# Optimization experiments

Measured on AMD Instinct MI355X. Metric: run time of the kernel, lower is better.

The kernel has to match this reference:

```python
import jax, jax.numpy as jnp
import numpy as np

N = 50000
E = 800000
IN_F, HID, OUT_F = 512, 256, 64
KEEP = 0.5  # Dropout(0.5)


def setup_inputs() -> dict:
    key = jax.random.key(0)
    ks = jax.random.split(key, 7)
    X = jax.random.normal(ks[0], (N, IN_F), dtype=jnp.float32)
    # Xavier-uniform-style init for the two layer weights
    lim1 = float(np.sqrt(6.0 / (IN_F + HID)))
    lim2 = float(np.sqrt(6.0 / (HID + OUT_F)))
    W1 = jax.random.uniform(ks[1], (IN_F, HID), jnp.float32, -lim1, lim1)
    W2 = jax.random.uniform(ks[2], (HID, OUT_F), jnp.float32, -lim2, lim2)
    a_row = jnp.sort(jax.random.randint(ks[3], (E,), 0, N)).astype(jnp.int64)
    a_col = jax.random.randint(ks[4], (E,), 0, N).astype(jnp.int64)
    a_val = jax.random.uniform(ks[5], (E,), jnp.float32)
    drop_mask = jax.random.randint(ks[6], (N, HID), 0, 2).astype(jnp.int32)
    return {"X": X, "W1": W1, "W2": W2, "a_row": a_row, "a_col": a_col,
            "a_val": a_val, "drop_mask": drop_mask}


def _spmm(a_row, a_col, a_val, dense):
    # A @ dense where A is [N, N] sparse in COO form: gather + weighted segment-sum
    msgs = a_val[:, None] * dense[a_col]          # [E, d]
    return jax.ops.segment_sum(msgs, a_row, num_segments=N)


def reference(X, W1, W2, a_row, a_col, a_val, drop_mask):
    # layer 1: feature transform + neighbor aggregation
    h = _spmm(a_row, a_col, a_val, X @ W1)        # [N, HID]
    h = jax.nn.relu(h)
    h = h * drop_mask.astype(h.dtype) * (1.0 / KEEP)  # Dropout(0.5), train mode
    # layer 2
    out = _spmm(a_row, a_col, a_val, h @ W2)      # [N, OUT_F]
    return jax.nn.log_softmax(out, axis=1)
```

## Files before the change

### kernel.cpp

```cpp
#include <hip/hip_runtime.h>
#include <hip/hip_bf16.h>
#include <math.h>

#define NN   50000
#define EE   800000
#define INF  512
#define HIDF 256
#define OUTF 64
#define MTILES (NN/16)

using short8 = __attribute__((ext_vector_type(8))) short;
using short4v = __attribute__((ext_vector_type(4))) short;
using f32x4  = __attribute__((ext_vector_type(4))) float;

static __device__ __forceinline__ short f2bf(float f){
  unsigned u = __builtin_bit_cast(unsigned, f);
  u += 0x7fff + ((u >> 16) & 1);
  return (short)(u >> 16);
}
static __device__ __forceinline__ float bf2f(short s){
  unsigned u = ((unsigned)(unsigned short)s) << 16;
  return __builtin_bit_cast(float, u);
}

__global__ void k_prep(const int* __restrict__ a_row, int* __restrict__ row_ptr,
                       const float* __restrict__ W1, short* __restrict__ W1p,
                       const float* __restrict__ W2, short* __restrict__ W2bT){
  int b = blockIdx.x, tid = threadIdx.x;
  if (b < 196){
    int i = b * 256 + tid;
    if (i > NN) return;
    int lo = 0, hi = EE;
    while (lo < hi){ int mid = (lo + hi) >> 1; if (a_row[mid] < i) lo = mid + 1; else hi = mid; }
    row_ptr[i] = lo;
  } else if (b < 708){
    int idx = (b - 196) * 256 + tid;
    int k = idx >> 8, col = idx & 255;
    int kk = k >> 5, k2 = k & 31;
    W1p[((kk << 8) + col) * 32 + k2] = f2bf(W1[idx]);
  } else {
    int idx = (b - 708) * 256 + tid;
    int k = idx >> 6, n = idx & 63;
    W2bT[n * HIDF + k] = f2bf(W2[idx]);
  }
}

__global__ __launch_bounds__(128) void k_gemm1(const float* __restrict__ X,
                                               const short* __restrict__ W1p,
                                               short* __restrict__ XW1b){
  int wave = threadIdx.x >> 6, lane = threadIdx.x & 63;
  int l16 = lane & 15, quad = lane >> 4;
  int m0 = blockIdx.x * 64 + wave * 32;
  int r0 = min(m0 + l16, NN - 1);
  int r1 = min(m0 + 16 + l16, NN - 1);
  const float* arow0 = X + (size_t)r0 * INF + quad * 8;
  const float* arow1 = X + (size_t)r1 * INF + quad * 8;

  f32x4 acc0[16], acc1[16];
  #pragma unroll
  for (int t = 0; t < 16; t++){ acc0[t] = (f32x4){0.f,0.f,0.f,0.f}; acc1[t] = (f32x4){0.f,0.f,0.f,0.f}; }

  for (int kk = 0; kk < INF/32; kk++){
    const float4* ap0 = (const float4*)(arow0 + kk * 32);
    const float4* ap1 = (const float4*)(arow1 + kk * 32);
    float4 a00 = ap0[0], a01 = ap0[1];
    float4 a10 = ap1[0], a11 = ap1[1];
    short8 af0, af1;
    af0[0]=f2bf(a00.x); af0[1]=f2bf(a00.y); af0[2]=f2bf(a00.z); af0[3]=f2bf(a00.w);
    af0[4]=f2bf(a01.x); af0[5]=f2bf(a01.y); af0[6]=f2bf(a01.z); af0[7]=f2bf(a01.w);
    af1[0]=f2bf(a10.x); af1[1]=f2bf(a10.y); af1[2]=f2bf(a10.z); af1[3]=f2bf(a10.w);
    af1[4]=f2bf(a11.x); af1[5]=f2bf(a11.y); af1[6]=f2bf(a11.z); af1[7]=f2bf(a11.w);

    const short* bchunk = W1p + kk * (256*32);
    #pragma unroll
    for (int nt = 0; nt < 16; nt++){
      short8 bf = *(const short8*)(bchunk + (nt*16 + l16) * 32 + quad * 8);
      acc0[nt] = __builtin_amdgcn_mfma_f32_16x16x32_bf16(af0, bf, acc0[nt], 0, 0, 0);
      acc1[nt] = __builtin_amdgcn_mfma_f32_16x16x32_bf16(af1, bf, acc1[nt], 0, 0, 0);
    }
  }
  #pragma unroll
  for (int nt = 0; nt < 16; nt++){
    int col = nt*16 + l16;
    #pragma unroll
    for (int r = 0; r < 4; r++){
      int row0 = m0 + quad*4 + r;
      int row1 = m0 + 16 + quad*4 + r;
      if (row0 < NN) XW1b[(size_t)row0 * HIDF + col] = f2bf(acc0[nt][r]);
      if (row1 < NN) XW1b[(size_t)row1 * HIDF + col] = f2bf(acc1[nt][r]);
    }
  }
}

__global__ __launch_bounds__(256) void k_spmm1(const int* __restrict__ row_ptr,
                                               const int* __restrict__ a_col,
                                               const float* __restrict__ a_val,
                                               const short* __restrict__ XW1b,
                                               const int* __restrict__ drop_mask,
                                               short* __restrict__ hb){
  int wave = threadIdx.x >> 6, lane = threadIdx.x & 63;
  int r = blockIdx.x * 4 + wave;
  int s = row_ptr[r], e = row_ptr[r+1];
  int g = lane >> 3;
  int c8 = lane & 7;
  float acc[32];
  #pragma unroll
  for (int j = 0; j < 32; j++) acc[j] = 0.f;

  int i = s + g;
  for (; i + 8 < e; i += 16){
    float v0 = a_val[i];     int c0 = a_col[i];
    float v1 = a_val[i+8];   int c1 = a_col[i+8];
    const short* p0 = XW1b + (size_t)c0 * HIDF + c8 * 32;
    const short* p1 = XW1b + (size_t)c1 * HIDF + c8 * 32;
    short8 x0[4], x1[4];
    #pragma unroll
    for (int q = 0; q < 4; q++){ x0[q] = *(const short8*)(p0 + q*8); }
    #pragma unroll
    for (int q = 0; q < 4; q++){ x1[q] = *(const short8*)(p1 + q*8); }
    #pragma unroll
    for (int q = 0; q < 4; q++)
      #pragma unroll
      for (int j = 0; j < 8; j++){
        acc[q*8+j] += v0 * bf2f(x0[q][j]);
        acc[q*8+j] += v1 * bf2f(x1[q][j]);
      }
  }
  for (; i < e; i += 8){
    float v = a_val[i];  int c = a_col[i];
    const short* p = XW1b + (size_t)c * HIDF + c8 * 32;
    #pragma unroll
    for (int q = 0; q < 4; q++){
      short8 x = *(const short8*)(p + q*8);
      #pragma unroll
      for (int j = 0; j < 8; j++) acc[q*8+j] += v * bf2f(x[j]);
    }
  }
  #pragma unroll
  for (int j = 0; j < 32; j++){
    acc[j] += __shfl_xor(acc[j], 8);
    acc[j] += __shfl_xor(acc[j], 16);
    acc[j] += __shfl_xor(acc[j], 32);
  }
  if (lane < 8){
    const int* dm = drop_mask + (size_t)r * HIDF + c8 * 32;
    short* hp = hb + (size_t)r * HIDF + c8 * 32;
    #pragma unroll
    for (int q = 0; q < 4; q++){
      short8 o;
      #pragma unroll
      for (int j = 0; j < 8; j++)
        o[j] = f2bf(fmaxf(acc[q*8+j], 0.f) * (float)dm[q*8+j] * 2.0f);
      *(short8*)(hp + q*8) = o;
    }
  }
}

__global__ __launch_bounds__(256) void k_gemm2(const short* __restrict__ A,
                                               const short* __restrict__ BT,
                                               short* __restrict__ C){
  int wave = threadIdx.x >> 6, lane = threadIdx.x & 63;
  int tile_m = blockIdx.x * 4 + wave;
  if (tile_m >= MTILES) return;
  int m0 = tile_m * 16, l16 = lane & 15, quad = lane >> 4;

  f32x4 acc[4];
  #pragma unroll
  for (int t = 0; t < 4; t++) acc[t] = (f32x4){0.f,0.f,0.f,0.f};

  const short* ar = A + (size_t)(m0 + l16) * HIDF + quad * 8;
  for (int kk = 0; kk < HIDF/32; kk++){
    short8 af = *(const short8*)(ar + kk * 32);
    #pragma unroll
    for (int nt = 0; nt < 4; nt++){
      short8 bf = *(const short8*)(BT + (size_t)(nt*16 + l16) * HIDF + kk*32 + quad*8);
      acc[nt] = __builtin_amdgcn_mfma_f32_16x16x32_bf16(af, bf, acc[nt], 0, 0, 0);
    }
  }
  #pragma unroll
  for (int nt = 0; nt < 4; nt++){
    int col = nt*16 + l16;
    #pragma unroll
    for (int r = 0; r < 4; r++)
      C[(size_t)(m0 + quad*4 + r) * OUTF + col] = f2bf(acc[nt][r]);
  }
}

__global__ __launch_bounds__(256) void k_spmm2_lsm(const int* __restrict__ row_ptr,
                                                   const int* __restrict__ a_col,
                                                   const float* __restrict__ a_val,
                                                   const short* __restrict__ HW2b,
                                                   float* __restrict__ out){
  int wave = threadIdx.x >> 6, lane = threadIdx.x & 63;
  int r = blockIdx.x * 4 + wave;
  int s = row_ptr[r], e = row_ptr[r+1];
  int g = lane >> 3;
  int c8 = lane & 7;
  float acc[8];
  #pragma unroll
  for (int j = 0; j < 8; j++) acc[j] = 0.f;

  int i = s + g;
  for (; i + 8 < e; i += 16){
    float v0 = a_val[i];    int c0 = a_col[i];
    float v1 = a_val[i+8];  int c1 = a_col[i+8];
    short8 x0 = *(const short8*)(HW2b + (size_t)c0 * OUTF + c8 * 8);
    short8 x1 = *(const short8*)(HW2b + (size_t)c1 * OUTF + c8 * 8);
    #pragma unroll
    for (int j = 0; j < 8; j++){ acc[j] += v0 * bf2f(x0[j]); acc[j] += v1 * bf2f(x1[j]); }
  }
  for (; i < e; i += 8){
    float v = a_val[i];  int c = a_col[i];
    short8 x = *(const short8*)(HW2b + (size_t)c * OUTF + c8 * 8);
    #pragma unroll
    for (int j = 0; j < 8; j++) acc[j] += v * bf2f(x[j]);
  }
  #pragma unroll
  for (int j = 0; j < 8; j++){
    acc[j] += __shfl_xor(acc[j], 8);
    acc[j] += __shfl_xor(acc[j], 16);
    acc[j] += __shfl_xor(acc[j], 32);
  }
  float m = acc[0];
  #pragma unroll
  for (int j = 1; j < 8; j++) m = fmaxf(m, acc[j]);
  #pragma unroll
  for (int o = 1; o <= 4; o <<= 1) m = fmaxf(m, __shfl_xor(m, o));
  float ssum = 0.f;
  #pragma unroll
  for (int j = 0; j < 8; j++) ssum += expf(acc[j] - m);
  #pragma unroll
  for (int o = 1; o <= 4; o <<= 1) ssum += __shfl_xor(ssum, o);
  float ls = logf(ssum);
  if (lane < 8){
    float4 o0 = { acc[0]-m-ls, acc[1]-m-ls, acc[2]-m-ls, acc[3]-m-ls };
    float4 o1 = { acc[4]-m-ls, acc[5]-m-ls, acc[6]-m-ls, acc[7]-m-ls };
    float* op = out + (size_t)r * OUTF + c8 * 8;
    *(float4*)(op)     = o0;
    *(float4*)(op + 4) = o1;
  }
}

extern "C" void kernel_launch(void* const* d_in, const int* in_sizes, int n_in,
                              void* d_out, int out_size, void* d_ws, size_t ws_size,
                              hipStream_t stream) {
  const float* X      = (const float*)d_in[0];
  const float* W1     = (const float*)d_in[1];
  const float* W2     = (const float*)d_in[2];
  const int*   a_row  = (const int*)d_in[3];
  const int*   a_col  = (const int*)d_in[4];
  const float* a_val  = (const float*)d_in[5];
  const int*   drop   = (const int*)d_in[6];
  float*       out    = (float*)d_out;

  char* ws = (char*)d_ws;
  int*   row_ptr = (int*)  (ws);
  short* W1p     = (short*)(ws + 200704);
  short* W2bT    = (short*)(ws + 462848);
  short* XW1b    = (short*)(ws + 495616);
  short* hb      = (short*)(ws + 26095616);
  short* HW2b    = (short*)(ws + 51695616);

  k_prep<<<772, 256, 0, stream>>>(a_row, row_ptr, W1, W1p, W2, W2bT);
  k_gemm1<<<(NN + 63)/64, 128, 0, stream>>>(X, W1p, XW1b);
  k_spmm1<<<NN/4, 256, 0, stream>>>(row_ptr, a_col, a_val, XW1b, drop, hb);
  k_gemm2<<<(MTILES + 3)/4, 256, 0, stream>>>(hb, W2bT, HW2b);
  k_spmm2_lsm<<<NN/4, 256, 0, stream>>>(row_ptr, a_col, a_val, HW2b, out);
}
```

Before: 355.6 us.

## Slice feature matrices column-wise so SpMM gathers stay cache-resident per slice

The GEMM outputs are now stored in column-sliced layouts: XW1 as 8 slices of 32 columns and HW2 as 4 slices of 16 columns, each contiguous over all nodes. The SpMM kernels assign each block to one slice and 16 rows, so a slice's gather working set (about 3.2 MB or 1.6 MB) is small enough to stay in L2/LLC during random neighbor gathers. Log-softmax moves into a separate pass over the fp32 output. The cost is re-reading row_ptr, a_col and a_val once per slice, one extra kernel launch, and an extra read and write of the output.

```diff
diff --git a/kernel.cpp b/kernel.cpp
--- a/kernel.cpp
+++ b/kernel.cpp
@@ -47,7 +47,7 @@
 
 __global__ __launch_bounds__(128) void k_gemm1(const float* __restrict__ X,
                                                const short* __restrict__ W1p,
-                                               short* __restrict__ XW1b){
+                                               short* __restrict__ XW1s){
   int wave = threadIdx.x >> 6, lane = threadIdx.x & 63;
   int l16 = lane & 15, quad = lane >> 4;
   int m0 = blockIdx.x * 64 + wave * 32;
@@ -81,13 +81,14 @@
   }
   #pragma unroll
   for (int nt = 0; nt < 16; nt++){
-    int col = nt*16 + l16;
+    int s = nt >> 1;
+    short* base = XW1s + (size_t)s * NN * 32 + (nt & 1) * 16 + l16;
     #pragma unroll
     for (int r = 0; r < 4; r++){
       int row0 = m0 + quad*4 + r;
       int row1 = m0 + 16 + quad*4 + r;
-      if (row0 < NN) XW1b[(size_t)row0 * HIDF + col] = f2bf(acc0[nt][r]);
-      if (row1 < NN) XW1b[(size_t)row1 * HIDF + col] = f2bf(acc1[nt][r]);
+      if (row0 < NN) base[(size_t)row0 * 32] = f2bf(acc0[nt][r]);
+      if (row1 < NN) base[(size_t)row1 * 32] = f2bf(acc1[nt][r]);
     }
   }
 }
@@ -95,70 +96,60 @@
 __global__ __launch_bounds__(256) void k_spmm1(const int* __restrict__ row_ptr,
                                                const int* __restrict__ a_col,
                                                const float* __restrict__ a_val,
-                                               const short* __restrict__ XW1b,
+                                               const short* __restrict__ XW1s,
                                                const int* __restrict__ drop_mask,
                                                short* __restrict__ hb){
-  int wave = threadIdx.x >> 6, lane = threadIdx.x & 63;
-  int r = blockIdx.x * 4 + wave;
-  int s = row_ptr[r], e = row_ptr[r+1];
-  int g = lane >> 3;
-  int c8 = lane & 7;
-  float acc[32];
-  #pragma unroll
-  for (int j = 0; j < 32; j++) acc[j] = 0.f;
-
-  int i = s + g;
-  for (; i + 8 < e; i += 16){
+  int s  = blockIdx.x & 7;
+  int rg = blockIdx.x >> 3;
+  int wave = threadIdx.x >> 6, lane = threadIdx.x & 63;
+  int row_local = lane >> 4;
+  int grp = (lane >> 2) & 3;
+  int q   = lane & 3;
+  int r = rg * 16 + wave * 4 + row_local;
+  int es = row_ptr[r], ee = row_ptr[r+1];
+  const short* Xs = XW1s + (size_t)s * NN * 32 + q * 8;
+
+  float acc[8] = {0,0,0,0,0,0,0,0};
+  int i = es + grp;
+  for (; i + 4 < ee; i += 8){
     float v0 = a_val[i];     int c0 = a_col[i];
-    float v1 = a_val[i+8];   int c1 = a_col[i+8];
-    const short* p0 = XW1b + (size_t)c0 * HIDF + c8 * 32;
-    const short* p1 = XW1b + (size_t)c1 * HIDF + c8 * 32;
-    short8 x0[4], x1[4];
-    #pragma unroll
-    for (int q = 0; q < 4; q++){ x0[q] = *(const short8*)(p0 + q*8); }
-    #pragma unroll
-    for (int q = 0; q < 4; q++){ x1[q] = *(const short8*)(p1 + q*8); }
-    #pragma unroll
-    for (int q = 0; q < 4; q++)
-      #pragma unroll
-      for (int j = 0; j < 8; j++){
-        acc[q*8+j] += v0 * bf2f(x0[q][j]);
-        acc[q*8+j] += v1 * bf2f(x1[q][j]);
-      }
-  }
-  for (; i < e; i += 8){
+    float v1 = a_val[i+4];   int c1 = a_col[i+4];
+    short8 x0 = *(const short8*)(Xs + (size_t)c0 * 32);
+    short8 x1 = *(const short8*)(Xs + (size_t)c1 * 32);
+    #pragma unroll
+    for (int j = 0; j < 8; j++){ acc[j] += v0 * bf2f(x0[j]); acc[j] += v1 * bf2f(x1[j]); }
+  }
+  for (; i < ee; i += 4){
     float v = a_val[i];  int c = a_col[i];
-    const short* p = XW1b + (size_t)c * HIDF + c8 * 32;
-    #pragma unroll
-    for (int q = 0; q < 4; q++){
-      short8 x = *(const short8*)(p + q*8);
-      #pragma unroll
-      for (int j = 0; j < 8; j++) acc[q*8+j] += v * bf2f(x[j]);
-    }
-  }
-  #pragma unroll
-  for (int j = 0; j < 32; j++){
+    short8 x = *(const short8*)(Xs + (size_t)c * 32);
+    #pragma unroll
+    for (int j = 0; j < 8; j++) acc[j] += v * bf2f(x[j]);
+  }
+  #pragma unroll
+  for (int j = 0; j < 8; j++){
+    acc[j] += __shfl_xor(acc[j], 4);
     acc[j] += __shfl_xor(acc[j], 8);
-    acc[j] += __shfl_xor(acc[j], 16);
-    acc[j] += __shfl_xor(acc[j], 32);
-  }
-  if (lane < 8){
-    const int* dm = drop_mask + (size_t)r * HIDF + c8 * 32;
-    short* hp = hb + (size_t)r * HIDF + c8 * 32;
-    #pragma unroll
-    for (int q = 0; q < 4; q++){
-      short8 o;
-      #pragma unroll
-      for (int j = 0; j < 8; j++)
-        o[j] = f2bf(fmaxf(acc[q*8+j], 0.f) * (float)dm[q*8+j] * 2.0f);
-      *(short8*)(hp + q*8) = o;
-    }
+  }
+  if (grp == 0){
+    const int* dm = drop_mask + (size_t)r * HIDF + s * 32 + q * 8;
+    int4 d0 = *(const int4*)(dm);
+    int4 d1 = *(const int4*)(dm + 4);
+    short8 o;
+    o[0] = f2bf(fmaxf(acc[0],0.f) * (float)d0.x * 2.0f);
+    o[1] = f2bf(fmaxf(acc[1],0.f) * (float)d0.y * 2.0f);
+    o[2] = f2bf(fmaxf(acc[2],0.f) * (float)d0.z * 2.0f);
+    o[3] = f2bf(fmaxf(acc[3],0.f) * (float)d0.w * 2.0f);
+    o[4] = f2bf(fmaxf(acc[4],0.f) * (float)d1.x * 2.0f);
+    o[5] = f2bf(fmaxf(acc[5],0.f) * (float)d1.y * 2.0f);
+    o[6] = f2bf(fmaxf(acc[6],0.f) * (float)d1.z * 2.0f);
+    o[7] = f2bf(fmaxf(acc[7],0.f) * (float)d1.w * 2.0f);
+    *(short8*)(hb + (size_t)r * HIDF + s * 32 + q * 8) = o;
   }
 }
 
 __global__ __launch_bounds__(256) void k_gemm2(const short* __restrict__ A,
                                                const short* __restrict__ BT,
-                                               short* __restrict__ C){
+                                               short* __restrict__ HW2s){
   int wave = threadIdx.x >> 6, lane = threadIdx.x & 63;
   int tile_m = blockIdx.x * 4 + wave;
   if (tile_m >= MTILES) return;
@@ -179,66 +170,66 @@
   }
   #pragma unroll
   for (int nt = 0; nt < 4; nt++){
-    int col = nt*16 + l16;
+    short* base = HW2s + (size_t)nt * NN * 16 + l16;
     #pragma unroll
     for (int r = 0; r < 4; r++)
-      C[(size_t)(m0 + quad*4 + r) * OUTF + col] = f2bf(acc[nt][r]);
-  }
-}
-
-__global__ __launch_bounds__(256) void k_spmm2_lsm(const int* __restrict__ row_ptr,
-                                                   const int* __restrict__ a_col,
-                                                   const float* __restrict__ a_val,
-                                                   const short* __restrict__ HW2b,
-                                                   float* __restrict__ out){
+      base[(size_t)(m0 + quad*4 + r) * 16] = f2bf(acc[nt][r]);
+  }
+}
+
+__global__ __launch_bounds__(256) void k_spmm2(const int* __restrict__ row_ptr,
+                                               const int* __restrict__ a_col,
+                                               const float* __restrict__ a_val,
+                                               const short* __restrict__ HW2s,
+                                               float* __restrict__ out){
+  int t  = blockIdx.x & 3;
+  int rg = blockIdx.x >> 2;
+  int wave = threadIdx.x >> 6, lane = threadIdx.x & 63;
+  int row_local = lane >> 4;
+  int grp = (lane >> 2) & 3;
+  int q   = lane & 3;
+  int r = rg * 16 + wave * 4 + row_local;
+  int es = row_ptr[r], ee = row_ptr[r+1];
+  const short* Hs = HW2s + (size_t)t * NN * 16 + q * 4;
+
+  float acc[4] = {0,0,0,0};
+  int i = es + grp;
+  for (; i + 4 < ee; i += 8){
+    float v0 = a_val[i];     int c0 = a_col[i];
+    float v1 = a_val[i+4];   int c1 = a_col[i+4];
+    short4v x0 = *(const short4v*)(Hs + (size_t)c0 * 16);
+    short4v x1 = *(const short4v*)(Hs + (size_t)c1 * 16);
+    #pragma unroll
+    for (int j = 0; j < 4; j++){ acc[j] += v0 * bf2f(x0[j]); acc[j] += v1 * bf2f(x1[j]); }
+  }
+  for (; i < ee; i += 4){
+    float v = a_val[i];  int c = a_col[i];
+    short4v x = *(const short4v*)(Hs + (size_t)c * 16);
+    #pragma unroll
+    for (int j = 0; j < 4; j++) acc[j] += v * bf2f(x[j]);
+  }
+  #pragma unroll
+  for (int j = 0; j < 4; j++){
+    acc[j] += __shfl_xor(acc[j], 4);
+    acc[j] += __shfl_xor(acc[j], 8);
+  }
+  if (grp == 0){
+    float4 o4 = { acc[0], acc[1], acc[2], acc[3] };
+    *(float4*)(out + (size_t)r * OUTF + t * 16 + q * 4) = o4;
+  }
+}
+
+__global__ __launch_bounds__(256) void k_lsm(float* __restrict__ out){
   int wave = threadIdx.x >> 6, lane = threadIdx.x & 63;
   int r = blockIdx.x * 4 + wave;
-  int s = row_ptr[r], e = row_ptr[r+1];
-  int g = lane >> 3;
-  int c8 = lane & 7;
-  float acc[8];
-  #pragma unroll
-  for (int j = 0; j < 8; j++) acc[j] = 0.f;
-
-  int i = s + g;
-  for (; i + 8 < e; i += 16){
-    float v0 = a_val[i];    int c0 = a_col[i];
-    float v1 = a_val[i+8];  int c1 = a_col[i+8];
-    short8 x0 = *(const short8*)(HW2b + (size_t)c0 * OUTF + c8 * 8);
-    short8 x1 = *(const short8*)(HW2b + (size_t)c1 * OUTF + c8 * 8);
-    #pragma unroll
-    for (int j = 0; j < 8; j++){ acc[j] += v0 * bf2f(x0[j]); acc[j] += v1 * bf2f(x1[j]); }
-  }
-  for (; i < e; i += 8){
-    float v = a_val[i];  int c = a_col[i];
-    short8 x = *(const short8*)(HW2b + (size_t)c * OUTF + c8 * 8);
-    #pragma unroll
-    for (int j = 0; j < 8; j++) acc[j] += v * bf2f(x[j]);
-  }
-  #pragma unroll
-  for (int j = 0; j < 8; j++){
-    acc[j] += __shfl_xor(acc[j], 8);
-    acc[j] += __shfl_xor(acc[j], 16);
-    acc[j] += __shfl_xor(acc[j], 32);
-  }
-  float m = acc[0];
-  #pragma unroll
-  for (int j = 1; j < 8; j++) m = fmaxf(m, acc[j]);
-  #pragma unroll
-  for (int o = 1; o <= 4; o <<= 1) m = fmaxf(m, __shfl_xor(m, o));
-  float ssum = 0.f;
-  #pragma unroll
-  for (int j = 0; j < 8; j++) ssum += expf(acc[j] - m);
-  #pragma unroll
-  for (int o = 1; o <= 4; o <<= 1) ssum += __shfl_xor(ssum, o);
-  float ls = logf(ssum);
-  if (lane < 8){
-    float4 o0 = { acc[0]-m-ls, acc[1]-m-ls, acc[2]-m-ls, acc[3]-m-ls };
-    float4 o1 = { acc[4]-m-ls, acc[5]-m-ls, acc[6]-m-ls, acc[7]-m-ls };
-    float* op = out + (size_t)r * OUTF + c8 * 8;
-    *(float4*)(op)     = o0;
-    *(float4*)(op + 4) = o1;
-  }
+  float x = out[(size_t)r * OUTF + lane];
+  float m = x;
+  #pragma unroll
+  for (int o = 1; o <= 32; o <<= 1) m = fmaxf(m, __shfl_xor(m, o));
+  float ssum = expf(x - m);
+  #pragma unroll
+  for (int o = 1; o <= 32; o <<= 1) ssum += __shfl_xor(ssum, o);
+  out[(size_t)r * OUTF + lane] = x - m - logf(ssum);
 }
 
 extern "C" void kernel_launch(void* const* d_in, const int* in_sizes, int n_in,
@@ -257,13 +248,14 @@
   int*   row_ptr = (int*)  (ws);
   short* W1p     = (short*)(ws + 200704);
   short* W2bT    = (short*)(ws + 462848);
-  short* XW1b    = (short*)(ws + 495616);
+  short* XW1s    = (short*)(ws + 495616);
   short* hb      = (short*)(ws + 26095616);
-  short* HW2b    = (short*)(ws + 51695616);
+  short* HW2s    = (short*)(ws + 51695616);
 
   k_prep<<<772, 256, 0, stream>>>(a_row, row_ptr, W1, W1p, W2, W2bT);
-  k_gemm1<<<(NN + 63)/64, 128, 0, stream>>>(X, W1p, XW1b);
-  k_spmm1<<<NN/4, 256, 0, stream>>>(row_ptr, a_col, a_val, XW1b, drop, hb);
-  k_gemm2<<<(MTILES + 3)/4, 256, 0, stream>>>(hb, W2bT, HW2b);
-  k_spmm2_lsm<<<NN/4, 256, 0, stream>>>(row_ptr, a_col, a_val, HW2b, out);
-}
+  k_gemm1<<<(NN + 63)/64, 128, 0, stream>>>(X, W1p, XW1s);
+  k_spmm1<<<8 * (NN/16), 256, 0, stream>>>(row_ptr, a_col, a_val, XW1s, drop, hb);
+  k_gemm2<<<(MTILES + 3)/4, 256, 0, stream>>>(hb, W2bT, HW2s);
+  k_spmm2<<<4 * (NN/16), 256, 0, stream>>>(row_ptr, a_col, a_val, HW2s, out);
+  k_lsm<<<NN/4, 256, 0, stream>>>(out);
+}
```

Result: slower. 363.5 us (+2.2%).
